# Kernel optimization log

Measured on AMD Instinct MI355X. Metric: run time of the kernel, lower is better.

## Reference

```python
import jax, jax.numpy as jnp
import numpy as np

B, Q, S, C, D = 32, 128, 2048, 1024, 1024  # batch, query steps, ctx steps, ctx dim, query dim


def setup_inputs() -> dict:
    key = jax.random.key(0)
    k1, k2, k3, k4 = jax.random.split(key, 4)
    context = jax.random.normal(k1, (B, S, C), jnp.float32)
    query = jax.random.normal(k2, (Q, B, D), jnp.float32)
    context_mask = jax.random.randint(k3, (B, S), 0, 2).astype(bool)  # True = masked out
    weights = jax.random.normal(k4, (C, D), jnp.float32)  # nn.Parameter(...).normal_()
    return {"context": context, "query": query, "context_mask": context_mask, "weights": weights}


def reference(context, query, context_mask, weights):
    # Bilinear scores: (context @ W) bmm query^T -> [B, Q, S]; transposed to [Q, B, S]
    # for the per-query-step scan. temp = 1.0 so no rescaling.
    scores = jnp.einsum('bsc,cd,qbd->qbs', context, weights, query)
    neg_inf = jnp.asarray(-jnp.inf, scores.dtype)

    def step(accum, score):  # accum, score: [B, S]
        adj = jnp.where(context_mask, neg_inf, score - accum)  # coverage-adjusted score
        a = jax.nn.softmax(adj, axis=-1)
        return accum + a, a

    accum0 = jnp.zeros((B, S), scores.dtype)
    accum, attention = jax.lax.scan(step, accum0, scores)  # attention: [Q, B, S]

    # compute_composition=True branch; torch returns attention permuted to [Q, B, S],
    # accum [B, 1, S], composition [Q, B, C].
    composition = jnp.einsum('qbs,bsc->qbc', attention, context)
    return attention, accum[:, None, :], composition
```

## Files before the change

### kernel.cpp

```cpp
#include <hip/hip_runtime.h>

#define B_ 32
#define Q_ 128
#define S_ 2048
#define C_ 1024
#define D_ 1024

typedef __attribute__((ext_vector_type(8))) short bf16x8;
typedef __attribute__((ext_vector_type(4))) float f32x4;
typedef __attribute__((ext_vector_type(4))) unsigned int u32x4;

static __device__ __forceinline__ unsigned short f2bf(float f) {
  unsigned int u = __float_as_uint(f);
  u = (u + 0x7FFFu + ((u >> 16) & 1u)) >> 16;
  return (unsigned short)u;
}
static __device__ __forceinline__ float bf2f(unsigned short h) {
  return __uint_as_float(((unsigned int)h) << 16);
}

static __device__ __forceinline__ void gl_lds16(const void* g, void* l) {
  __builtin_amdgcn_global_load_lds(
      (const __attribute__((address_space(1))) unsigned int*)g,
      (__attribute__((address_space(3))) unsigned int*)l, 16, 0, 0);
}

template <int CTRL>
static __device__ __forceinline__ float dpp_ror(float v) {
  return __uint_as_float((unsigned int)__builtin_amdgcn_update_dpp(
      0, (int)__float_as_uint(v), CTRL, 0xf, 0xf, false));
}

static __device__ __forceinline__ void split8(const f32x4 x0, const f32x4 x1,
                                              bf16x8& hi, bf16x8& lo) {
  u32x4 h, l;
#pragma unroll
  for (int p = 0; p < 2; ++p) {
    const unsigned int a0 = __float_as_uint(x0[2 * p]);
    const unsigned int a1 = __float_as_uint(x0[2 * p + 1]);
    h[p] = __builtin_amdgcn_perm(a1, a0, 0x07060302u);
    const float r0 = x0[2 * p]     - __uint_as_float(a0 & 0xffff0000u);
    const float r1 = x0[2 * p + 1] - __uint_as_float(a1 & 0xffff0000u);
    l[p] = __builtin_amdgcn_perm(__float_as_uint(r1), __float_as_uint(r0), 0x07060302u);
  }
#pragma unroll
  for (int p = 0; p < 2; ++p) {
    const unsigned int a0 = __float_as_uint(x1[2 * p]);
    const unsigned int a1 = __float_as_uint(x1[2 * p + 1]);
    h[2 + p] = __builtin_amdgcn_perm(a1, a0, 0x07060302u);
    const float r0 = x1[2 * p]     - __uint_as_float(a0 & 0xffff0000u);
    const float r1 = x1[2 * p + 1] - __uint_as_float(a1 & 0xffff0000u);
    l[2 + p] = __builtin_amdgcn_perm(__float_as_uint(r1), __float_as_uint(r0), 0x07060302u);
  }
  hi = __builtin_bit_cast(bf16x8, h);
  lo = __builtin_bit_cast(bf16x8, l);
}

template <bool FUSE>
__global__ __launch_bounds__(256, 2)
void gemm_f32(const float* __restrict__ Aip, const float* __restrict__ Bip,
              float* __restrict__ outp, int K,
              long aBatch, long bBatch, long outBatch,
              long aRstride, long bRstride, long outRstride, int remapQB,
              unsigned short* __restrict__ fuseOut, long fuseRstride) {
  extern __shared__ char smem[];
  float* sA = (float*)smem;
  float* sB = sA + 8192;

  const int tid = threadIdx.x;
  const int lane = tid & 63;
  const int w = tid >> 6;
  const int wr = w >> 1;
  const int wc = w & 1;
  const int m0 = blockIdx.y * 128;
  const int n0 = blockIdx.x * 128;
  const int bz = blockIdx.z;
  const int frow = lane & 15;
  const int cc = lane >> 4;

  const float* Af = Aip + (long)bz * aBatch;
  const float* Bf = Bip + (long)bz * bBatch;

  f32x4 acc[4][4];
#pragma unroll
  for (int i = 0; i < 4; ++i)
#pragma unroll
    for (int j = 0; j < 4; ++j) acc[i][j] = (f32x4){0.f, 0.f, 0.f, 0.f};

  auto STAGE = [&](int ktt, int bufi) {
#pragma unroll
    for (int i = 0; i < 4; ++i) {
      const int rr = (w * 4 + i) * 8 + (lane >> 3);
      const int cs = (lane & 7) ^ (rr & 7);
      gl_lds16(Af + (long)(m0 + rr) * aRstride + ktt + cs * 4,
               sA + bufi * 4096 + (w * 4 + i) * 256);
    }
#pragma unroll
    for (int i = 0; i < 4; ++i) {
      const int rr = (w * 4 + i) * 8 + (lane >> 3);
      const int cs = (lane & 7) ^ (rr & 7);
      gl_lds16(Bf + (long)(n0 + rr) * bRstride + ktt + cs * 4,
               sB + bufi * 4096 + (w * 4 + i) * 256);
    }
  };

  const int nt = K >> 5;
  STAGE(0, 0);
  STAGE(32, 1);

  for (int t = 0; t < nt; ++t) {
    if (t + 1 < nt) { asm volatile("s_waitcnt vmcnt(8)" ::: "memory"); }
    else            { asm volatile("s_waitcnt vmcnt(0)" ::: "memory"); }
    __builtin_amdgcn_sched_barrier(0);
    asm volatile("s_barrier" ::: "memory");

    const float* sAb = sA + (t & 1) * 4096;
    const float* sBb = sB + (t & 1) * 4096;

    bf16x8 ah[4], al[4], bh[4], bl[4];
#pragma unroll
    for (int i = 0; i < 4; ++i) {
      const int row = wr * 64 + i * 16 + frow;
      const int c0 = ((cc * 2) ^ (row & 7)) << 2;
      const int c1 = ((cc * 2 + 1) ^ (row & 7)) << 2;
      split8(*(const f32x4*)(sAb + row * 32 + c0),
             *(const f32x4*)(sAb + row * 32 + c1), ah[i], al[i]);
    }
#pragma unroll
    for (int j = 0; j < 4; ++j) {
      const int row = wc * 64 + j * 16 + frow;
      const int c0 = ((cc * 2) ^ (row & 7)) << 2;
      const int c1 = ((cc * 2 + 1) ^ (row & 7)) << 2;
      split8(*(const f32x4*)(sBb + row * 32 + c0),
             *(const f32x4*)(sBb + row * 32 + c1), bh[j], bl[j]);
    }
#pragma unroll
    for (int i = 0; i < 4; ++i)
#pragma unroll
      for (int j = 0; j < 4; ++j) {
        acc[i][j] = __builtin_amdgcn_mfma_f32_16x16x32_bf16(ah[i], bh[j], acc[i][j], 0, 0, 0);
        acc[i][j] = __builtin_amdgcn_mfma_f32_16x16x32_bf16(ah[i], bl[j], acc[i][j], 0, 0, 0);
        acc[i][j] = __builtin_amdgcn_mfma_f32_16x16x32_bf16(al[i], bh[j], acc[i][j], 0, 0, 0);
      }

    if constexpr (FUSE) {
      const int k = lane & 31;
      const int nb = w * 32 + ((lane >> 5) << 4);
      unsigned short vals[16];
#pragma unroll
      for (int i = 0; i < 16; ++i) {
        const int row = nb + i;
        vals[i] = f2bf(sBb[row * 32 + (((k >> 2) ^ (row & 7)) << 2) + (k & 3)]);
      }
      unsigned short* dst = fuseOut + ((long)bz * K + t * 32 + k) * fuseRstride + n0 + nb;
      *(bf16x8*)(dst + 0) = *(const bf16x8*)(vals + 0);
      *(bf16x8*)(dst + 8) = *(const bf16x8*)(vals + 8);
    }

    asm volatile("s_barrier" ::: "memory");
    if (t + 2 < nt) STAGE((t + 2) * 32, t & 1);
  }

  float* out = outp + (long)bz * outBatch;
#pragma unroll
  for (int i = 0; i < 4; ++i) {
#pragma unroll
    for (int rr = 0; rr < 4; ++rr) {
      const int grow = m0 + wr * 64 + i * 16 + ((lane >> 4) << 2) + rr;
      const long orow = remapQB ? ((long)(grow & 31) * 128 + (grow >> 5)) : (long)grow;
      float* orp = out + orow * outRstride;
#pragma unroll
      for (int j = 0; j < 4; ++j) {
        const int col = n0 + wc * 64 + j * 16 + (lane & 15);
        orp[col] = acc[i][j][rr];
      }
    }
  }
}

__global__ __launch_bounds__(256, 2)
void gemm_bf16(const unsigned short* __restrict__ Aip, const unsigned short* __restrict__ Bip,
               float* __restrict__ outp, int K,
               long aBatch, long bBatch, long outBatch,
               long aRstride, long bRstride, long outRstride) {
  extern __shared__ char smem[];
  unsigned short* sA = (unsigned short*)smem;
  unsigned short* sB = sA + 16384;

  const int tid = threadIdx.x;
  const int lane = tid & 63;
  const int w = tid >> 6;
  const int wr = w >> 1;
  const int wc = w & 1;
  const int m0 = blockIdx.y * 128;
  const int n0 = blockIdx.x * 128;
  const int bz = blockIdx.z;
  const int frow = lane & 15;
  const int cc = lane >> 4;

  const unsigned short* Ab = Aip + (long)bz * aBatch;
  const unsigned short* Bb = Bip + (long)bz * bBatch;

  f32x4 acc[4][4];
#pragma unroll
  for (int i = 0; i < 4; ++i)
#pragma unroll
    for (int j = 0; j < 4; ++j) acc[i][j] = (f32x4){0.f, 0.f, 0.f, 0.f};

  auto STAGE = [&](int ktt, int bufi) {
#pragma unroll
    for (int i = 0; i < 4; ++i) {
      const int rr = (w * 4 + i) * 8 + (lane >> 3);
      const int cs = (lane & 7) ^ (rr & 7);
      gl_lds16(Ab + (long)(m0 + rr) * aRstride + ktt + cs * 8,
               sA + bufi * 8192 + (w * 4 + i) * 512);
    }
#pragma unroll
    for (int i = 0; i < 4; ++i) {
      const int rr = (w * 4 + i) * 8 + (lane >> 3);
      const int cs = (lane & 7) ^ (rr & 7);
      gl_lds16(Bb + (long)(n0 + rr) * bRstride + ktt + cs * 8,
               sB + bufi * 8192 + (w * 4 + i) * 512);
    }
  };

  const int nt = K >> 6;
  STAGE(0, 0);
  STAGE(64, 1);

  for (int t = 0; t < nt; ++t) {
    if (t + 1 < nt) { asm volatile("s_waitcnt vmcnt(8)" ::: "memory"); }
    else            { asm volatile("s_waitcnt vmcnt(0)" ::: "memory"); }
    __builtin_amdgcn_sched_barrier(0);
    asm volatile("s_barrier" ::: "memory");

    const unsigned short* sAb = sA + (t & 1) * 8192;
    const unsigned short* sBb = sB + (t & 1) * 8192;

#pragma unroll
    for (int kk = 0; kk < 2; ++kk) {
      bf16x8 ah[4], bh[4];
#pragma unroll
      for (int i = 0; i < 4; ++i) {
        const int row = wr * 64 + i * 16 + frow;
        const int ch = kk * 4 + cc;
        ah[i] = *(const bf16x8*)((const char*)sAb + row * 128 + ((ch ^ (row & 7)) << 4));
      }
#pragma unroll
      for (int j = 0; j < 4; ++j) {
        const int row = wc * 64 + j * 16 + frow;
        const int ch = kk * 4 + cc;
        bh[j] = *(const bf16x8*)((const char*)sBb + row * 128 + ((ch ^ (row & 7)) << 4));
      }
#pragma unroll
      for (int i = 0; i < 4; ++i)
#pragma unroll
        for (int j = 0; j < 4; ++j)
          acc[i][j] = __builtin_amdgcn_mfma_f32_16x16x32_bf16(ah[i], bh[j], acc[i][j], 0, 0, 0);
    }

    asm volatile("s_barrier" ::: "memory");
    if (t + 2 < nt) STAGE((t + 2) * 64, t & 1);
  }

  float* out = outp + (long)bz * outBatch;
#pragma unroll
  for (int i = 0; i < 4; ++i) {
#pragma unroll
    for (int rr = 0; rr < 4; ++rr) {
      const int grow = m0 + wr * 64 + i * 16 + ((lane >> 4) << 2) + rr;
      float* orp = out + (long)grow * outRstride;
#pragma unroll
      for (int j = 0; j < 4; ++j) {
        const int col = n0 + wc * 64 + j * 16 + (lane & 15);
        orp[col] = acc[i][j][rr];
      }
    }
  }
}

template <int VM>
static __device__ __forceinline__ void scan_row(
    float* __restrict__ attn, unsigned short* __restrict__ attnb,
    int b, int q, int lane, int wid, int s0,
    const bool* msk, float* acc, f32x4& buf, float2 (&red)[2][8]) {
  const float L2E = 1.4426950408889634f;

  if constexpr (VM == 1)      asm volatile("s_waitcnt vmcnt(1)" ::: "memory");
  else if constexpr (VM == 3) asm volatile("s_waitcnt vmcnt(3)" ::: "memory");
  else                        asm volatile("s_waitcnt vmcnt(5)" ::: "memory");
  __builtin_amdgcn_sched_barrier(0);

  float adj[4];
#pragma unroll
  for (int j = 0; j < 4; ++j)
    adj[j] = msk[j] ? -1e30f : (buf[j] - acc[j]);

  int pr = q + 2; if (pr > Q_ - 1) pr = Q_ - 1;
  const float* pp = attn + ((long)(pr * B_ + b)) * S_ + s0;
  asm volatile("global_load_dwordx4 %0, %1, off"
               : "=&v"(buf)
               : "v"(pp), "v"(adj[0]), "v"(adj[1]), "v"(adj[2]), "v"(adj[3])
               : "memory");

  float lm = fmaxf(fmaxf(adj[0], adj[1]), fmaxf(adj[2], adj[3]));
  lm = fmaxf(lm, dpp_ror<0x121>(lm));
  lm = fmaxf(lm, dpp_ror<0x122>(lm));
  lm = fmaxf(lm, dpp_ror<0x124>(lm));
  lm = fmaxf(lm, dpp_ror<0x128>(lm));
  lm = fmaxf(lm, __shfl_xor(lm, 16));
  lm = fmaxf(lm, __shfl_xor(lm, 32));

  float e[4];
#pragma unroll
  for (int j = 0; j < 4; ++j) {
    const float x = exp2f((adj[j] - lm) * L2E);
    e[j] = msk[j] ? 0.f : x;
  }

  float ls = (e[0] + e[1]) + (e[2] + e[3]);
  ls += dpp_ror<0x121>(ls);
  ls += dpp_ror<0x122>(ls);
  ls += dpp_ror<0x124>(ls);
  ls += dpp_ror<0x128>(ls);
  ls += __shfl_xor(ls, 16);
  ls += __shfl_xor(ls, 32);

  const int p = q & 1;
  if (lane == 0) red[p][wid] = make_float2(lm, ls);
  asm volatile("s_waitcnt lgkmcnt(0)\n\ts_barrier" ::: "memory");

  const float2 v0 = red[p][0], v1 = red[p][1], v2 = red[p][2], v3 = red[p][3];
  const float2 v4 = red[p][4], v5 = red[p][5], v6 = red[p][6], v7 = red[p][7];
  const float M = fmaxf(fmaxf(fmaxf(v0.x, v1.x), fmaxf(v2.x, v3.x)),
                        fmaxf(fmaxf(v4.x, v5.x), fmaxf(v6.x, v7.x)));
  const float tot = v0.y * exp2f((v0.x - M) * L2E) + v1.y * exp2f((v1.x - M) * L2E) +
                    v2.y * exp2f((v2.x - M) * L2E) + v3.y * exp2f((v3.x - M) * L2E) +
                    v4.y * exp2f((v4.x - M) * L2E) + v5.y * exp2f((v5.x - M) * L2E) +
                    v6.y * exp2f((v6.x - M) * L2E) + v7.y * exp2f((v7.x - M) * L2E);
  const float scale = exp2f((lm - M) * L2E) / tot;

  f32x4 av;
#pragma unroll
  for (int j = 0; j < 4; ++j) {
    av[j] = e[j] * scale;
    acc[j] += av[j];
  }
  *(f32x4*)(attn + ((long)(q * B_ + b)) * S_ + s0) = av;
  uint2 pk;
  pk.x = (unsigned int)f2bf(av[0]) | ((unsigned int)f2bf(av[1]) << 16);
  pk.y = (unsigned int)f2bf(av[2]) | ((unsigned int)f2bf(av[3]) << 16);
  *(uint2*)(attnb + ((long)b * Q_ + q) * S_ + s0) = pk;
}

__global__ __launch_bounds__(512)
void scan_kernel(const int* __restrict__ mask, float* __restrict__ attn,
                 float* __restrict__ accum_out, unsigned short* __restrict__ attnb) {
  const int b = blockIdx.x;
  const int tid = threadIdx.x;
  const int lane = tid & 63;
  const int wid = tid >> 6;
  const int s0 = tid * 4;

  __shared__ float2 red[2][8];

  const int4 mk = *(const int4*)(mask + (long)b * S_ + s0);
  const bool msk[4] = {mk.x != 0, mk.y != 0, mk.z != 0, mk.w != 0};
  asm volatile("" :: "v"(mk.x), "v"(mk.y), "v"(mk.z), "v"(mk.w));

  float acc[4] = {0.f, 0.f, 0.f, 0.f};

  f32x4 bufE, bufO;
  const float* p0 = attn + (long)b * S_ + s0;
  asm volatile("global_load_dwordx4 %0, %1, off" : "=&v"(bufE) : "v"(p0) : "memory");
  const float* p1 = attn + ((long)(B_ + b)) * S_ + s0;
  asm volatile("global_load_dwordx4 %0, %1, off" : "=&v"(bufO) : "v"(p1) : "memory");

  scan_row<1>(attn, attnb, b, 0, lane, wid, s0, msk, acc, bufE, red);
  scan_row<3>(attn, attnb, b, 1, lane, wid, s0, msk, acc, bufO, red);
  for (int q = 2; q < Q_; q += 2) {
    scan_row<5>(attn, attnb, b, q,     lane, wid, s0, msk, acc, bufE, red);
    scan_row<5>(attn, attnb, b, q + 1, lane, wid, s0, msk, acc, bufO, red);
  }

  f32x4 a4;
#pragma unroll
  for (int j = 0; j < 4; ++j) a4[j] = acc[j];
  *(f32x4*)(accum_out + (long)b * S_ + s0) = a4;
}

extern "C" void kernel_launch(void* const* d_in, const int* in_sizes, int n_in,
                              void* d_out, int out_size, void* d_ws, size_t ws_size,
                              hipStream_t stream) {
  const float* ctx   = (const float*)d_in[0];
  const float* query = (const float*)d_in[1];
  const int*   mask  = (const int*)d_in[2];
  const float* W     = (const float*)d_in[3];

  float* out = (float*)d_out;
  float* attn = out;
  float* accum_out = out + (size_t)Q_ * B_ * S_;
  float* comp = accum_out + (size_t)B_ * S_;

  char* ws = (char*)d_ws;
  float* qw = (float*)ws;
  unsigned short* ctxT  = (unsigned short*)(ws + (size_t)16 * 1024 * 1024);
  unsigned short* attnb = (unsigned short*)(ws + (size_t)16 * 1024 * 1024 +
                                            (size_t)B_ * C_ * S_ * 2);

  gemm_f32<false><<<dim3(C_ / 128, (Q_ * B_) / 128, 1), 256, 65536, stream>>>(
      query, W, qw, D_, 0L, 0L, 0L, (long)D_, (long)D_, (long)C_, 1, nullptr, 0L);

  gemm_f32<true><<<dim3(S_ / 128, 1, B_), 256, 65536, stream>>>(
      qw, ctx, attn, C_, (long)Q_ * C_, (long)S_ * C_, (long)S_,
      (long)C_, (long)C_, (long)B_ * S_, 0, ctxT, (long)S_);

  scan_kernel<<<B_, 512, 0, stream>>>(mask, attn, accum_out, attnb);

  gemm_bf16<<<dim3(C_ / 128, 1, B_), 256, 65536, stream>>>(
      attnb, ctxT, comp, S_, (long)Q_ * S_, (long)C_ * S_, (long)C_,
      (long)S_, (long)S_, (long)B_ * C_);
}
```

Baseline: 319.8 us.

## Use a provisional max from the next row to shorten the softmax scan step

Each scan step now shifts its exponentials by a row maximum computed during the previous step. That maximum comes from the next row's scores minus the not-yet-updated accumulator, so it is never below the true maximum. This removes the dependent max reduction and the per-wave exp rescaling from the critical path of every serial step, leaving one fused sum/max exchange per barrier. In exchange, the next row's load must complete earlier (a tighter vmcnt wait), which reduces prefetch slack. An extra startup reduction and barrier are also added.

```diff
diff --git a/kernel.cpp b/kernel.cpp
--- a/kernel.cpp
+++ b/kernel.cpp
@@ -279,16 +279,17 @@
   }
 }
 
-template <int VM>
+template <int VMA, int VMB>
 static __device__ __forceinline__ void scan_row(
     float* __restrict__ attn, unsigned short* __restrict__ attnb,
     int b, int q, int lane, int wid, int s0,
-    const bool* msk, float* acc, f32x4& buf, float2 (&red)[2][8]) {
+    const bool* msk, float* acc, f32x4& buf, const f32x4& bufNext,
+    float& Mprov, float2 (&red)[2][8]) {
   const float L2E = 1.4426950408889634f;
 
-  if constexpr (VM == 1)      asm volatile("s_waitcnt vmcnt(1)" ::: "memory");
-  else if constexpr (VM == 3) asm volatile("s_waitcnt vmcnt(3)" ::: "memory");
-  else                        asm volatile("s_waitcnt vmcnt(5)" ::: "memory");
+  if constexpr (VMA == 1)      asm volatile("s_waitcnt vmcnt(1)" ::: "memory");
+  else if constexpr (VMA == 3) asm volatile("s_waitcnt vmcnt(3)" ::: "memory");
+  else                         asm volatile("s_waitcnt vmcnt(5)" ::: "memory");
   __builtin_amdgcn_sched_barrier(0);
 
   float adj[4];
@@ -303,18 +304,10 @@
                : "v"(pp), "v"(adj[0]), "v"(adj[1]), "v"(adj[2]), "v"(adj[3])
                : "memory");
 
-  float lm = fmaxf(fmaxf(adj[0], adj[1]), fmaxf(adj[2], adj[3]));
-  lm = fmaxf(lm, dpp_ror<0x121>(lm));
-  lm = fmaxf(lm, dpp_ror<0x122>(lm));
-  lm = fmaxf(lm, dpp_ror<0x124>(lm));
-  lm = fmaxf(lm, dpp_ror<0x128>(lm));
-  lm = fmaxf(lm, __shfl_xor(lm, 16));
-  lm = fmaxf(lm, __shfl_xor(lm, 32));
-
   float e[4];
 #pragma unroll
   for (int j = 0; j < 4; ++j) {
-    const float x = exp2f((adj[j] - lm) * L2E);
+    const float x = exp2f((adj[j] - Mprov) * L2E);
     e[j] = msk[j] ? 0.f : x;
   }
 
@@ -326,19 +319,31 @@
   ls += __shfl_xor(ls, 16);
   ls += __shfl_xor(ls, 32);
 
+  if constexpr (VMB == 1) asm volatile("s_waitcnt vmcnt(1)" ::: "memory");
+  else                    asm volatile("s_waitcnt vmcnt(3)" ::: "memory");
+  __builtin_amdgcn_sched_barrier(0);
+  float ap[4];
+#pragma unroll
+  for (int j = 0; j < 4; ++j)
+    ap[j] = msk[j] ? -1e30f : (bufNext[j] - acc[j]);
+  float lmp = fmaxf(fmaxf(ap[0], ap[1]), fmaxf(ap[2], ap[3]));
+  lmp = fmaxf(lmp, dpp_ror<0x121>(lmp));
+  lmp = fmaxf(lmp, dpp_ror<0x122>(lmp));
+  lmp = fmaxf(lmp, dpp_ror<0x124>(lmp));
+  lmp = fmaxf(lmp, dpp_ror<0x128>(lmp));
+  lmp = fmaxf(lmp, __shfl_xor(lmp, 16));
+  lmp = fmaxf(lmp, __shfl_xor(lmp, 32));
+
   const int p = q & 1;
-  if (lane == 0) red[p][wid] = make_float2(lm, ls);
+  if (lane == 0) red[p][wid] = make_float2(ls, lmp);
   asm volatile("s_waitcnt lgkmcnt(0)\n\ts_barrier" ::: "memory");
 
   const float2 v0 = red[p][0], v1 = red[p][1], v2 = red[p][2], v3 = red[p][3];
   const float2 v4 = red[p][4], v5 = red[p][5], v6 = red[p][6], v7 = red[p][7];
-  const float M = fmaxf(fmaxf(fmaxf(v0.x, v1.x), fmaxf(v2.x, v3.x)),
-                        fmaxf(fmaxf(v4.x, v5.x), fmaxf(v6.x, v7.x)));
-  const float tot = v0.y * exp2f((v0.x - M) * L2E) + v1.y * exp2f((v1.x - M) * L2E) +
-                    v2.y * exp2f((v2.x - M) * L2E) + v3.y * exp2f((v3.x - M) * L2E) +
-                    v4.y * exp2f((v4.x - M) * L2E) + v5.y * exp2f((v5.x - M) * L2E) +
-                    v6.y * exp2f((v6.x - M) * L2E) + v7.y * exp2f((v7.x - M) * L2E);
-  const float scale = exp2f((lm - M) * L2E) / tot;
+  const float tot = ((v0.x + v1.x) + (v2.x + v3.x)) + ((v4.x + v5.x) + (v6.x + v7.x));
+  const float Mn = fmaxf(fmaxf(fmaxf(v0.y, v1.y), fmaxf(v2.y, v3.y)),
+                         fmaxf(fmaxf(v4.y, v5.y), fmaxf(v6.y, v7.y)));
+  const float scale = 1.0f / tot;
 
   f32x4 av;
 #pragma unroll
@@ -351,6 +356,8 @@
   pk.x = (unsigned int)f2bf(av[0]) | ((unsigned int)f2bf(av[1]) << 16);
   pk.y = (unsigned int)f2bf(av[2]) | ((unsigned int)f2bf(av[3]) << 16);
   *(uint2*)(attnb + ((long)b * Q_ + q) * S_ + s0) = pk;
+
+  Mprov = Mn;
 }
 
 __global__ __launch_bounds__(512)
@@ -376,11 +383,32 @@
   const float* p1 = attn + ((long)(B_ + b)) * S_ + s0;
   asm volatile("global_load_dwordx4 %0, %1, off" : "=&v"(bufO) : "v"(p1) : "memory");
 
-  scan_row<1>(attn, attnb, b, 0, lane, wid, s0, msk, acc, bufE, red);
-  scan_row<3>(attn, attnb, b, 1, lane, wid, s0, msk, acc, bufO, red);
+  float Mprov;
+  {
+    asm volatile("s_waitcnt vmcnt(1)" ::: "memory");
+    __builtin_amdgcn_sched_barrier(0);
+    float a0[4];
+#pragma unroll
+    for (int j = 0; j < 4; ++j) a0[j] = msk[j] ? -1e30f : bufE[j];
+    float lm = fmaxf(fmaxf(a0[0], a0[1]), fmaxf(a0[2], a0[3]));
+    lm = fmaxf(lm, dpp_ror<0x121>(lm));
+    lm = fmaxf(lm, dpp_ror<0x122>(lm));
+    lm = fmaxf(lm, dpp_ror<0x124>(lm));
+    lm = fmaxf(lm, dpp_ror<0x128>(lm));
+    lm = fmaxf(lm, __shfl_xor(lm, 16));
+    lm = fmaxf(lm, __shfl_xor(lm, 32));
+    if (lane == 0) red[1][wid] = make_float2(0.f, lm);
+    asm volatile("s_waitcnt lgkmcnt(0)\n\ts_barrier" ::: "memory");
+    Mprov = red[1][0].y;
+#pragma unroll
+    for (int w2 = 1; w2 < 8; ++w2) Mprov = fmaxf(Mprov, red[1][w2].y);
+  }
+
+  scan_row<1, 1>(attn, attnb, b, 0, lane, wid, s0, msk, acc, bufE, bufO, Mprov, red);
+  scan_row<3, 3>(attn, attnb, b, 1, lane, wid, s0, msk, acc, bufO, bufE, Mprov, red);
   for (int q = 2; q < Q_; q += 2) {
-    scan_row<5>(attn, attnb, b, q,     lane, wid, s0, msk, acc, bufE, red);
-    scan_row<5>(attn, attnb, b, q + 1, lane, wid, s0, msk, acc, bufO, red);
+    scan_row<5, 3>(attn, attnb, b, q,     lane, wid, s0, msk, acc, bufE, bufO, Mprov, red);
+    scan_row<5, 3>(attn, attnb, b, q + 1, lane, wid, s0, msk, acc, bufO, bufE, Mprov, red);
   }
 
   f32x4 a4;
```

Result: faster. 286.4 us, median of 2 (-10.5%).
